# Optimization experiments

Measured on AMD Instinct MI355X. Metric: run time of the kernel, lower is better.

Reference implementation:

```python
import jax, jax.numpy as jnp
import numpy as np

B, W, F, D, H, L = 8, 256, 16, 128, 8, 4
DH = D                      # dim_head = embedding_dims in the original call
INNER = H * DH              # 1024
TIME_EMB = 4
SCALE = DH ** -0.5


def causal_conv(x, w, b, dilation):
    # x: [B, F, W]; w: [F, 1, K] depthwise (groups=F); left-pad (K-1)*dilation -> causal
    k = w.shape[-1]
    pad = (k - 1) * dilation
    y = jax.lax.conv_general_dilated(
        x, w, window_strides=(1,), padding=[(pad, 0)], rhs_dilation=(dilation,),
        dimension_numbers=("NCH", "OIH", "NCH"), feature_group_count=F)
    return y + b[None, :, None]


def sinusoidal_pe(length, d):
    pos = jnp.arange(length, dtype=jnp.float32)[:, None]
    div = jnp.exp(jnp.arange(0, d, 2, dtype=jnp.float32) * (-np.log(10000.0) / d))
    pe = jnp.zeros((length, d), dtype=jnp.float32)
    pe = pe.at[:, 0::2].set(jnp.sin(pos * div)).at[:, 1::2].set(jnp.cos(pos * div))
    return pe  # [W, D]


def layer_norm(x, g, b):
    m = x.mean(-1, keepdims=True)
    v = x.var(-1, keepdims=True)
    return (x - m) * jax.lax.rsqrt(v + 1e-5) * g + b


def vt_attention(x, g, bln, wqkv, wout, bout):
    # x: [B, W, F, D] -> PreNorm then dual-axis (variable + temporal) attention
    h = layer_norm(x, g, bln)
    qkv = h @ wqkv                                   # [B,W,F,3*INNER]
    q, k, v = jnp.split(qkv, 3, axis=-1)
    heads = lambda t: t.reshape(B, W, F, H, DH)
    q, k, v = heads(q) * SCALE, heads(k), heads(v)
    # variable attention: attend across the feature axis (per time step)
    av = jax.nn.softmax(jnp.einsum("bwihe,bwjhe->bwhij", q, k), axis=-1)  # [B,W,H,F,F]
    ov = jnp.einsum("bwhij,bwjhe->bwihe", av, v)
    # temporal attention: attend across the window axis (per variable)
    at = jax.nn.softmax(jnp.einsum("bifhe,bjfhe->bfhij", q, k), axis=-1)  # [B,F,H,W,W]
    ot = jnp.einsum("bfhij,bjfhe->bifhe", at, v)
    o = (ov + ot).reshape(B, W, F, INNER)
    return o @ wout + bout                            # [B,W,F,D]


def setup_inputs() -> dict:
    key = jax.random.key(0)
    ks = jax.random.split(key, 16)
    n = lambda k, shape, sc: jax.random.normal(k, shape, dtype=jnp.float32) * sc
    return {
        "x": jax.random.normal(ks[0], (B, W, F), dtype=jnp.float32),
        "conv_w1": n(ks[1], (F, 1, 4), 0.3), "conv_b1": jnp.zeros((F,), jnp.float32),
        "conv_w2": n(ks[2], (F, 1, 8), 0.2), "conv_b2": jnp.zeros((F,), jnp.float32),
        "conv_w3": n(ks[3], (F, 1, 16), 0.15), "conv_b3": jnp.zeros((F,), jnp.float32),
        "w_val": n(ks[4], (TIME_EMB, D), 0.3), "b_val": jnp.zeros((D,), jnp.float32),
        "ln_g": jnp.ones((L, D), jnp.float32), "ln_b": jnp.zeros((L, D), jnp.float32),
        "w_qkv": n(ks[5], (L, D, 3 * INNER), D ** -0.5),
        "w_out": n(ks[6], (L, INNER, D), INNER ** -0.5),
        "b_out": jnp.zeros((L, D), jnp.float32),
        "w_head": n(ks[7], (F * D, F), (F * D) ** -0.5),
        "b_head": jnp.zeros((F,), jnp.float32),
    }


def reference(x, conv_w1, conv_b1, conv_w2, conv_b2, conv_w3, conv_b3,
              w_val, b_val, ln_g, ln_b, w_qkv, w_out, b_out, w_head, b_head):
    xt = jnp.transpose(x, (0, 2, 1))                  # b w f -> b f w
    c1 = causal_conv(xt, conv_w1, conv_b1, 1)
    c2 = causal_conv(xt, conv_w2, conv_b2, 2)
    c3 = causal_conv(xt, conv_w3, conv_b3, 3)
    s = jnp.stack([xt, c1, c2, c3], axis=-1)          # [B,F,W,4]
    s = jnp.transpose(s, (0, 2, 1, 3))                # [B,W,F,4]
    e = s @ w_val + b_val                             # [B,W,F,D]
    pe = sinusoidal_pe(W, D)                          # [W,D] broadcast over b,f
    h = e + pe[None, :, None, :]
    for l in range(L):
        xo = vt_attention(h, ln_g[l], ln_b[l], w_qkv[l], w_out[l], b_out[l])
        h = xo + h                                    # residual
    out = h.reshape(B, W, F * D) @ w_head + b_head    # [B,W,F]
    return out
```

## Files before the change

kernel.cpp:

```cpp
#include <hip/hip_runtime.h>
#include <hip/hip_bf16.h>
#include <math.h>

#define BB 8
#define WW 256
#define FF 16
#define DD 128
#define HH 8
#define NTOK (BB*WW*FF)
#define SCALE 0.08838834764831845f
#define INV_D (1.0f/128.0f)
#define LN10K_D 0.07195578415606394f

typedef __hip_bfloat16 bf16;
typedef short bf16x8 __attribute__((ext_vector_type(8)));
typedef float f32x4 __attribute__((ext_vector_type(4)));

__device__ __forceinline__ float bf2f(bf16 x){ return __bfloat162float(x); }
__device__ __forceinline__ bf16 f2bf(float x){ return __float2bfloat16(x); }
__device__ __forceinline__ unsigned short bfbits(float x){ bf16 b = f2bf(x); return *(unsigned short*)&b; }
__device__ __forceinline__ float bits2f(unsigned short u){ bf16 b = *(bf16*)&u; return __bfloat162float(b); }

#define MFMA16 __builtin_amdgcn_mfma_f32_16x16x32_bf16


__global__ __launch_bounds__(256) void embed_kernel(
    const float* __restrict__ x,
    const float* __restrict__ w1, const float* __restrict__ b1,
    const float* __restrict__ w2, const float* __restrict__ b2,
    const float* __restrict__ w3, const float* __restrict__ b3,
    const float* __restrict__ wval, const float* __restrict__ bval,
    const float* __restrict__ g, const float* __restrict__ bln,
    float* __restrict__ h, bf16* __restrict__ hn)
{
    int bw = blockIdx.x;
    int b = bw >> 8, w = bw & 255;
    int tid = threadIdx.x;
    __shared__ float s[FF][4];
    __shared__ float hs[16*132];
    if (tid < 64) {
        int f = tid >> 2, t = tid & 3;
        const float* xb = x + (size_t)b*WW*FF + f;
        float v;
        if (t == 0) {
            v = xb[(size_t)w*FF];
        } else if (t == 1) {
            float acc = b1[f];
            #pragma unroll
            for (int kk = 0; kk < 4; kk++) { int t0 = w - (3-kk); if (t0 >= 0) acc += w1[f*4+kk]*xb[(size_t)t0*FF]; }
            v = acc;
        } else if (t == 2) {
            float acc = b2[f];
            #pragma unroll
            for (int kk = 0; kk < 8; kk++) { int t0 = w - (7-kk)*2; if (t0 >= 0) acc += w2[f*8+kk]*xb[(size_t)t0*FF]; }
            v = acc;
        } else {
            float acc = b3[f];
            #pragma unroll
            for (int kk = 0; kk < 16; kk++) { int t0 = w - (15-kk)*3; if (t0 >= 0) acc += w3[f*16+kk]*xb[(size_t)t0*FF]; }
            v = acc;
        }
        s[f][t] = v;
    }
    __syncthreads();
    #pragma unroll
    for (int r = 0; r < 8; r++) {
        int lin = r*256 + tid;
        int f = lin >> 7, d = lin & 127;
        float div = expf(-(float)(d & ~1) * LN10K_D);
        float arg = (float)w * div;
        float pe = (d & 1) ? cosf(arg) : sinf(arg);
        float e = bval[d] + pe;
        #pragma unroll
        for (int t = 0; t < 4; t++) e += s[f][t]*wval[t*128 + d];
        h[((size_t)bw*FF + f)*128 + d] = e;
        hs[f*132 + d] = e;
    }
    __syncthreads();
    int tok = tid >> 4, sub = tid & 15;
    float xv[8];
    #pragma unroll
    for (int e2 = 0; e2 < 8; e2++) xv[e2] = hs[tok*132 + sub*8 + e2];
    float s1 = 0.f, s2 = 0.f;
    #pragma unroll
    for (int e2 = 0; e2 < 8; e2++) { s1 += xv[e2]; s2 += xv[e2]*xv[e2]; }
    #pragma unroll
    for (int m = 1; m < 16; m <<= 1) { s1 += __shfl_xor(s1, m, 64); s2 += __shfl_xor(s2, m, 64); }
    float mean = s1*INV_D;
    float var  = s2*INV_D - mean*mean;
    float rs = rsqrtf(var + 1e-5f);
    union { uint4 u; unsigned short sh[8]; } ou;
    #pragma unroll
    for (int e2 = 0; e2 < 8; e2++) {
        int d = sub*8 + e2;
        ou.sh[e2] = bfbits((xv[e2]-mean)*rs*g[d] + bln[d]);
    }
    *(uint4*)(hn + ((size_t)bw*16 + tok)*128 + sub*8) = ou.u;
}

__global__ __launch_bounds__(256) void transpose_w(
    const float* __restrict__ wqkv, const float* __restrict__ wout,
    const float* __restrict__ wh,
    bf16* __restrict__ wqkvT, bf16* __restrict__ woutT, bf16* __restrict__ whT)
{
    __shared__ float tile[64][65];
    int bx = blockIdx.x, tid = threadIdx.x;
    const float* in; bf16* outp; int r0, c0, sin, sout, nmax;
    if (bx < 384) {
        int l = bx / 96, t = bx % 96;
        r0 = (t / 48)*64; c0 = (t % 48)*64;
        in = wqkv + (size_t)l*128*3072; outp = wqkvT + (size_t)l*3072*128;
        sin = 3072; sout = 128; nmax = 3072;
    } else if (bx < 512) {
        int j = bx - 384, l = j / 32, t = j % 32;
        r0 = (t / 2)*64; c0 = (t % 2)*64;
        in = wout + (size_t)l*1024*128; outp = woutT + (size_t)l*128*1024;
        sin = 128; sout = 1024; nmax = 128;
    } else {
        int t = bx - 512;
        r0 = t*64; c0 = 0;
        in = wh; outp = whT; sin = 16; sout = 2048; nmax = 16;
    }
    int rr = tid >> 2, cg = (tid & 3)*16;
    if (c0 + cg < nmax) {
        const float* src = in + (size_t)(r0 + rr)*sin + c0 + cg;
        #pragma unroll
        for (int i = 0; i < 4; i++)
            *(float4*)&tile[rr][cg + i*4] = *(const float4*)(src + i*4);
    }
    __syncthreads();
    int n = c0 + rr;
    if (n < nmax) {
        union { uint4 u[2]; unsigned short sh[16]; } o;
        #pragma unroll
        for (int e = 0; e < 16; e++) o.sh[e] = bfbits(tile[cg + e][rr]);
        bf16* dst = outp + (size_t)n*sout + r0 + cg;
        *(uint4*)dst = o.u[0];
        *(uint4*)(dst + 8) = o.u[1];
    }
}

__global__ __launch_bounds__(256) void qkv_mfma(
    const bf16* __restrict__ hn, const bf16* __restrict__ wT,
    bf16* __restrict__ q, bf16* __restrict__ k, bf16* __restrict__ v,
    int dummy)
{
    __shared__ __align__(16) unsigned short Cs[4][64][72];
    int tid = threadIdx.x;
    int lane = tid & 63, wave = tid >> 6;
    int quad = lane >> 4, l16 = lane & 15;
    int wm = wave >> 1, wn = wave & 1;
    int m0 = blockIdx.x * 128, n0 = blockIdx.y * 128;

    f32x4 acc[4][4];
    #pragma unroll
    for (int a = 0; a < 4; a++)
        #pragma unroll
        for (int c = 0; c < 4; c++) acc[a][c] = 0.f;

    #pragma unroll
    for (int kt = 0; kt < 4; kt++) {
        int ko = kt*32 + quad*8;
        bf16x8 af[4], bfr[4];
        #pragma unroll
        for (int tm = 0; tm < 4; tm++)
            af[tm] = *(const bf16x8*)(hn + (size_t)(m0 + wm*64 + tm*16 + l16)*128 + ko);
        #pragma unroll
        for (int tn = 0; tn < 4; tn++)
            bfr[tn] = *(const bf16x8*)(wT + (size_t)(n0 + wn*64 + tn*16 + l16)*128 + ko);
        #pragma unroll
        for (int tm = 0; tm < 4; tm++)
            #pragma unroll
            for (int tn = 0; tn < 4; tn++)
                acc[tm][tn] = MFMA16(af[tm], bfr[tn], acc[tm][tn], 0, 0, 0);
    }

    bf16* dst; int nrel; float scl; int isq;
    if (n0 < 1024)      { dst = q; nrel = n0;        scl = SCALE; isq = 1; }
    else if (n0 < 2048) { dst = k; nrel = n0 - 1024; scl = 1.0f;  isq = 0; }
    else                { dst = v; nrel = n0 - 2048; scl = 1.0f;  isq = 0; }

    #pragma unroll
    for (int tm = 0; tm < 4; tm++)
        #pragma unroll
        for (int tn = 0; tn < 4; tn++)
            #pragma unroll
            for (int r = 0; r < 4; r++)
                Cs[wave][tm*16 + quad*4 + r][tn*16 + l16] = bfbits(acc[tm][tn][r]*scl);

    if (isq) {
        #pragma unroll
        for (int p = 0; p < 8; p++) {
            int row = p*8 + (lane >> 3);
            int c8  = (lane & 7)*8;
            uint4 val = *(const uint4*)&Cs[wave][row][c8];
            size_t gaddr = (size_t)(m0 + wm*64 + row)*1024 + nrel + wn*64 + c8;
            *(uint4*)(dst + gaddr) = val;
        }
    } else {
        int hh = nrel >> 7;
        #pragma unroll
        for (int p = 0; p < 8; p++) {
            int row = p*8 + (lane >> 3);
            int c8  = (lane & 7)*8;
            uint4 val = *(const uint4*)&Cs[wave][row][c8];
            int tok = m0 + wm*64 + row;
            int bl = tok >> 12, w = (tok >> 4) & 255, f = tok & 15;
            int d  = wn*64 + c8;
            size_t gaddr = ((size_t)((bl*16 + f)*8 + hh) << 15) + (size_t)w*128 + d;
            *(uint4*)(dst + gaddr) = val;
        }
    }
}

__global__ __launch_bounds__(256) void tattn_mfma(
    const bf16* __restrict__ q, const bf16* __restrict__ k, const bf16* __restrict__ v,
    bf16* __restrict__ o)
{
    __shared__ __align__(16) unsigned short VsT[128*72];
    __shared__ __align__(16) unsigned short Ps[4][16][72];
    unsigned short* Os = VsT;
    unsigned int* VsTdw = (unsigned int*)VsT;

    int bx = blockIdx.x;
    int hh = bx & 7, it2 = (bx>>3) & 1, f = (bx>>4) & 15, bl = bx >> 8;
    int tid = threadIdx.x;
    int lane = tid & 63, wave = tid >> 6;
    int quad = lane >> 4, l16 = lane & 15;

    size_t baseQ = ((size_t)(bl*WW)*FF + f)*1024 + (size_t)hh*128;
    size_t baseK = (size_t)((bl*16 + f)*8 + hh) << 15;

    #pragma unroll 1
    for (int pass = 0; pass < 2; pass++) {
        int i0 = it2*128 + pass*64;

        bf16x8 af[4];
        {
            size_t qa = baseQ + (size_t)(i0 + wave*16 + l16)*16384;
            #pragma unroll
            for (int kt = 0; kt < 4; kt++)
                af[kt] = *(const bf16x8*)(q + qa + kt*32 + quad*8);
        }

        f32x4 oacc[8];
        #pragma unroll
        for (int t = 0; t < 8; t++) oacc[t] = 0.f;
        float m_run[4], l_run[4];
        #pragma unroll
        for (int r = 0; r < 4; r++) { m_run[r] = -1e30f; l_run[r] = 0.f; }

        #pragma unroll 1
        for (int jt = 0; jt < 4; jt++) {
            __syncthreads();
            #pragma unroll
            for (int p = 0; p < 2; p++) {
                int lin = p*256 + tid;
                int j2 = lin & 31;
                int c2 = (lin >> 5)*8;
                union { uint4 u; unsigned short sh[8]; } a, b;
                a.u = *(const uint4*)(v + baseK + (size_t)(jt*64 + 2*j2)*128 + c2);
                b.u = *(const uint4*)(v + baseK + (size_t)(jt*64 + 2*j2 + 1)*128 + c2);
                int col2 = (((2*j2) + (c2 & 56)) & 63) >> 1;
                #pragma unroll
                for (int e = 0; e < 8; e++)
                    VsTdw[(c2+e)*36 + col2] = (unsigned int)a.sh[e] | ((unsigned int)b.sh[e] << 16);
            }
            __syncthreads();

            f32x4 st[4];
            #pragma unroll
            for (int t = 0; t < 4; t++) st[t] = 0.f;
            #pragma unroll
            for (int t = 0; t < 4; t++) {
                size_t ja = baseK + (size_t)(jt*64 + t*16 + l16)*128;
                #pragma unroll
                for (int kt = 0; kt < 4; kt++) {
                    bf16x8 kf = *(const bf16x8*)(k + ja + kt*32 + quad*8);
                    st[t] = MFMA16(af[kt], kf, st[t], 0, 0, 0);
                }
            }

            float tmax[4];
            #pragma unroll
            for (int r = 0; r < 4; r++) tmax[r] = fmaxf(fmaxf(st[0][r], st[1][r]), fmaxf(st[2][r], st[3][r]));
            #pragma unroll
            for (int m = 1; m < 16; m <<= 1)
                #pragma unroll
                for (int r = 0; r < 4; r++) tmax[r] = fmaxf(tmax[r], __shfl_xor(tmax[r], m, 64));
            float alpha[4], rsum[4];
            #pragma unroll
            for (int r = 0; r < 4; r++) {
                float mnew = fmaxf(m_run[r], tmax[r]);
                alpha[r] = __expf(m_run[r] - mnew);
                m_run[r] = mnew;
                rsum[r] = 0.f;
            }
            #pragma unroll
            for (int t = 0; t < 4; t++)
                #pragma unroll
                for (int r = 0; r < 4; r++) {
                    float pp = __expf(st[t][r] - m_run[r]);
                    st[t][r] = pp;
                    rsum[r] += pp;
                }
            #pragma unroll
            for (int m = 1; m < 16; m <<= 1)
                #pragma unroll
                for (int r = 0; r < 4; r++) rsum[r] += __shfl_xor(rsum[r], m, 64);
            #pragma unroll
            for (int r = 0; r < 4; r++) l_run[r] = l_run[r]*alpha[r] + rsum[r];
            #pragma unroll
            for (int t = 0; t < 8; t++)
                #pragma unroll
                for (int r = 0; r < 4; r++) oacc[t][r] *= alpha[r];

            #pragma unroll
            for (int t = 0; t < 4; t++)
                #pragma unroll
                for (int r = 0; r < 4; r++)
                    Ps[wave][quad*4+r][t*16+l16] = bfbits(st[t][r]);

            #pragma unroll
            for (int kt2 = 0; kt2 < 2; kt2++) {
                int kbase = kt2*32 + quad*8;
                bf16x8 pf = *(const bf16x8*)&Ps[wave][l16][kbase];
                #pragma unroll
                for (int t = 0; t < 8; t++) {
                    int d = t*16 + l16;
                    int colstart = (kbase + (((d>>3)&7) << 3)) & 63;
                    bf16x8 vf = *(const bf16x8*)&VsT[d*72 + colstart];
                    oacc[t] = MFMA16(pf, vf, oacc[t], 0, 0, 0);
                }
            }
        }

        __syncthreads();
        float inv[4];
        #pragma unroll
        for (int r = 0; r < 4; r++) inv[r] = 1.f / l_run[r];
        #pragma unroll
        for (int t = 0; t < 8; t++)
            #pragma unroll
            for (int r = 0; r < 4; r++)
                Os[(wave*16 + quad*4 + r)*136 + t*16 + l16] = bfbits(oacc[t][r]*inv[r]);
        __syncthreads();
        #pragma unroll
        for (int r4 = 0; r4 < 4; r4++) {
            int row = r4*4 + quad;
            uint4 val = *(const uint4*)&Os[(wave*16 + row)*136 + l16*8];
            size_t gaddr = baseQ + (size_t)(i0 + wave*16 + row)*16384 + l16*8;
            *(uint4*)(o + gaddr) = val;
        }
    }
}

__global__ __launch_bounds__(256) void vproj_mfma(
    const bf16* __restrict__ q, const bf16* __restrict__ k, const bf16* __restrict__ v,
    const bf16* __restrict__ ot, const bf16* __restrict__ woT,
    const float* __restrict__ bo, float* __restrict__ h,
    bf16* __restrict__ hn, const float* __restrict__ gN, const float* __restrict__ bN,
    int donorm, int tokbase)
{
    __shared__ __align__(16) unsigned short VsT[1024*24];
    __shared__ __align__(16) unsigned short Ps[4][16][24];
    __shared__ float red2[4][16][2];
    unsigned short* Osum = VsT;
    unsigned int* VsTdw = (unsigned int*)VsT;

    int tid = threadIdx.x;
    int lane = tid & 63, wave = tid >> 6, quad = lane >> 4, l16 = lane & 15;
    int bl = blockIdx.x >> 8, w = blockIdx.x & 255;
    size_t base = (size_t)blockIdx.x * 16384;
    size_t woff = (size_t)w * 128;

    uint4 otpre[8];
    #pragma unroll
    for (int u = 0; u < 8; u++) {
        int lin = u*256 + tid;
        int fr = lin >> 7, dc = (lin & 127)*8;
        otpre[u] = *(const uint4*)(ot + base + (size_t)fr*1024 + dc);
    }

    #pragma unroll
    for (int p = 0; p < 4; p++) {
        int lin = p*256 + tid;
        int j2 = lin & 7;
        int d0 = (lin >> 3)*8;
        int hh2 = d0 >> 7, dd = d0 & 127;
        union { uint4 u; unsigned short sh[8]; } a, b;
        a.u = *(const uint4*)(v + (((size_t)((bl*16 + 2*j2  )*8 + hh2)) << 15) + woff + dd);
        b.u = *(const uint4*)(v + (((size_t)((bl*16 + 2*j2+1)*8 + hh2)) << 15) + woff + dd);
        #pragma unroll
        for (int e = 0; e < 8; e++)
            VsTdw[(d0+e)*12 + j2] = (unsigned int)a.sh[e] | ((unsigned int)b.sh[e] << 16);
    }
    __syncthreads();

    bf16x8 zf = {0,0,0,0,0,0,0,0};
    f32x4 oa[2][8];
    #pragma unroll
    for (int hi = 0; hi < 2; hi++) {
        int hh = wave*2 + hi;
        size_t hb = base + hh*128;

        f32x4 s = {0.f,0.f,0.f,0.f};
        size_t ka = (((size_t)((bl*16 + l16)*8 + hh)) << 15) + woff;
        #pragma unroll
        for (int kt = 0; kt < 4; kt++) {
            bf16x8 qf = *(const bf16x8*)(q + hb + (size_t)l16*1024 + kt*32 + quad*8);
            bf16x8 kf = *(const bf16x8*)(k + ka + kt*32 + quad*8);
            s = MFMA16(qf, kf, s, 0, 0, 0);
        }
        float p[4];
        #pragma unroll
        for (int r = 0; r < 4; r++) {
            float mxv = s[r];
            #pragma unroll
            for (int m = 1; m < 16; m <<= 1) mxv = fmaxf(mxv, __shfl_xor(mxv, m, 64));
            float e = __expf(s[r] - mxv);
            float smv = e;
            #pragma unroll
            for (int m = 1; m < 16; m <<= 1) smv += __shfl_xor(smv, m, 64);
            p[r] = e / smv;
        }
        #pragma unroll
        for (int r = 0; r < 4; r++) Ps[wave][quad*4+r][l16] = bfbits(p[r]);

        bf16x8 pf = zf;
        if (quad < 2) pf = *(const bf16x8*)&Ps[wave][l16][quad*8];
        #pragma unroll
        for (int dt = 0; dt < 8; dt++) oa[hi][dt] = 0.f;
        #pragma unroll
        for (int dt = 0; dt < 8; dt++) {
            bf16x8 vf = zf;
            if (quad < 2) vf = *(const bf16x8*)&VsT[(size_t)(hh*128 + dt*16 + l16)*24 + quad*8];
            oa[hi][dt] = MFMA16(pf, vf, oa[hi][dt], 0, 0, 0);
        }
    }

    __syncthreads();
    #pragma unroll
    for (int hi = 0; hi < 2; hi++) {
        int hh = wave*2 + hi;
        #pragma unroll
        for (int dt = 0; dt < 8; dt++)
            #pragma unroll
            for (int r = 0; r < 4; r++)
                Osum[(quad*4 + r)*1048 + hh*128 + dt*16 + l16] = bfbits(oa[hi][dt][r]);
    }
    __syncthreads();

    #pragma unroll
    for (int u = 0; u < 8; u++) {
        int lin = u*256 + tid;
        int fr = lin >> 7, dc = (lin & 127)*8;
        union { uint4 u4; unsigned short sh[8]; } a, bsh, wv;
        a.u4   = otpre[u];
        bsh.u4 = *(const uint4*)&Osum[fr*1048 + dc];
        #pragma unroll
        for (int e = 0; e < 8; e++)
            wv.sh[e] = bfbits(bits2f(a.sh[e]) + bits2f(bsh.sh[e]));
        *(uint4*)&Osum[fr*1048 + dc] = wv.u4;
    }
    __syncthreads();

    f32x4 pacc[2];
    pacc[0] = 0.f; pacc[1] = 0.f;
    #pragma unroll 4
    for (int kt2 = 0; kt2 < 32; kt2++) {
        bf16x8 af2 = *(const bf16x8*)&Osum[l16*1048 + kt2*32 + quad*8];
        #pragma unroll
        for (int nt = 0; nt < 2; nt++) {
            bf16x8 bfr = *(const bf16x8*)(woT + (size_t)(wave*32 + nt*16 + l16)*1024 + kt2*32 + quad*8);
            pacc[nt] = MFMA16(af2, bfr, pacc[nt], 0, 0, 0);
        }
    }

    int htok = tokbase + blockIdx.x*16;
    float hv[2][4];
    #pragma unroll
    for (int nt = 0; nt < 2; nt++) {
        int n = wave*32 + nt*16 + l16;
        float bias = bo[n];
        #pragma unroll
        for (int r = 0; r < 4; r++) {
            size_t idx = (size_t)(htok + quad*4 + r)*128 + n;
            float nv = h[idx] + pacc[nt][r] + bias;
            h[idx] = nv;
            hv[nt][r] = nv;
        }
    }

    if (donorm) {
        float s1[4], s2[4];
        #pragma unroll
        for (int r = 0; r < 4; r++) {
            s1[r] = hv[0][r] + hv[1][r];
            s2[r] = hv[0][r]*hv[0][r] + hv[1][r]*hv[1][r];
        }
        #pragma unroll
        for (int m = 1; m < 16; m <<= 1)
            #pragma unroll
            for (int r = 0; r < 4; r++) {
                s1[r] += __shfl_xor(s1[r], m, 64);
                s2[r] += __shfl_xor(s2[r], m, 64);
            }
        __syncthreads();
        if (l16 == 0) {
            #pragma unroll
            for (int r = 0; r < 4; r++) {
                red2[wave][quad*4+r][0] = s1[r];
                red2[wave][quad*4+r][1] = s2[r];
            }
        }
        __syncthreads();
        #pragma unroll
        for (int nt = 0; nt < 2; nt++) {
            int n = wave*32 + nt*16 + l16;
            float gn = gN[n], bn = bN[n];
            #pragma unroll
            for (int r = 0; r < 4; r++) {
                int t = quad*4 + r;
                float t1 = red2[0][t][0] + red2[1][t][0] + red2[2][t][0] + red2[3][t][0];
                float t2 = red2[0][t][1] + red2[1][t][1] + red2[2][t][1] + red2[3][t][1];
                float mean = t1*INV_D;
                float var  = t2*INV_D - mean*mean;
                float rsv = rsqrtf(var + 1e-5f);
                Osum[t*1048 + n] = bfbits((hv[nt][r]-mean)*rsv*gn + bn);
            }
        }
        __syncthreads();
        int row = tid >> 4, c8 = (tid & 15)*8;
        uint4 val = *(const uint4*)&Osum[row*1048 + c8];
        *(uint4*)(hn + (size_t)(htok + row)*128 + c8) = val;
    }
}

__global__ __launch_bounds__(256) void head_mfma(
    const float* __restrict__ h, const bf16* __restrict__ whT,
    const float* __restrict__ bh, float* __restrict__ out)
{
    __shared__ float sred[4][16][17];
    int tid = threadIdx.x;
    int lane = tid & 63, wave = tid >> 6, quad = lane >> 4, l16 = lane & 15;
    int bw0 = blockIdx.x * 16;
    const float* hrow = h + (size_t)(bw0 + l16)*2048 + wave*512;
    const bf16* wrow  = whT + (size_t)l16*2048 + wave*512;

    f32x4 acc = {0.f,0.f,0.f,0.f};
    #pragma unroll 4
    for (int kc = 0; kc < 16; kc++) {
        int ko = kc*32 + quad*8;
        float4 a0 = *(const float4*)(hrow + ko);
        float4 a1 = *(const float4*)(hrow + ko + 4);
        union { bf16x8 v; unsigned short sh[8]; } ua;
        ua.sh[0]=bfbits(a0.x); ua.sh[1]=bfbits(a0.y); ua.sh[2]=bfbits(a0.z); ua.sh[3]=bfbits(a0.w);
        ua.sh[4]=bfbits(a1.x); ua.sh[5]=bfbits(a1.y); ua.sh[6]=bfbits(a1.z); ua.sh[7]=bfbits(a1.w);
        bf16x8 bv = *(const bf16x8*)(wrow + ko);
        acc = MFMA16(ua.v, bv, acc, 0, 0, 0);
    }
    #pragma unroll
    for (int r = 0; r < 4; r++) sred[wave][quad*4+r][l16] = acc[r];
    __syncthreads();
    int i = tid >> 4, n = tid & 15;
    float s = bh[n] + sred[0][i][n] + sred[1][i][n] + sred[2][i][n] + sred[3][i][n];
    out[(size_t)(bw0 + i)*16 + n] = s;
}

extern "C" void kernel_launch(void* const* d_in, const int* in_sizes, int n_in,
                              void* d_out, int out_size, void* d_ws, size_t ws_size,
                              hipStream_t stream)
{
    const float* x    = (const float*)d_in[0];
    const float* w1   = (const float*)d_in[1];
    const float* b1   = (const float*)d_in[2];
    const float* w2   = (const float*)d_in[3];
    const float* b2   = (const float*)d_in[4];
    const float* w3   = (const float*)d_in[5];
    const float* b3   = (const float*)d_in[6];
    const float* wval = (const float*)d_in[7];
    const float* bval = (const float*)d_in[8];
    const float* lng  = (const float*)d_in[9];
    const float* lnb  = (const float*)d_in[10];
    const float* wqkv = (const float*)d_in[11];
    const float* wout = (const float*)d_in[12];
    const float* bout = (const float*)d_in[13];
    const float* wh   = (const float*)d_in[14];
    const float* bh   = (const float*)d_in[15];
    float* out = (float*)d_out;

    char* ws = (char*)d_ws;
    bf16*  wqkvT = (bf16*)ws;
    bf16*  woutT = (bf16*)(ws + 3145728);
    bf16*  whT   = (bf16*)(ws + 4194304);
    float* h     = (float*)(ws + 4259840);
    bf16*  hn    = (bf16*)(ws + 21037056);
    const size_t qoff = 29425664ull;

    int NBL = 1;
    if      (ws_size >= qoff + 8ull*4ull*8388608ull) NBL = 8;
    else if (ws_size >= qoff + 4ull*4ull*8388608ull) NBL = 4;
    else if (ws_size >= qoff + 2ull*4ull*8388608ull) NBL = 2;
    size_t bsz = (size_t)NBL * 8388608ull;
    bf16* q  = (bf16*)(ws + qoff);
    bf16* kk = (bf16*)(ws + qoff + bsz);
    bf16* vv = (bf16*)(ws + qoff + 2*bsz);
    bf16* oo = (bf16*)(ws + qoff + 3*bsz);

    transpose_w<<<544, 256, 0, stream>>>(wqkv, wout, wh, wqkvT, woutT, whT);
    embed_kernel<<<BB*WW, 256, 0, stream>>>(x, w1,b1, w2,b2, w3,b3, wval, bval,
                                            lng, lnb, h, hn);

    for (int l = 0; l < 4; l++) {
        const bf16* wqT_l = wqkvT + (size_t)l*3072*128;
        const bf16* woT_l = woutT + (size_t)l*128*1024;
        const float* bo_l = bout + l*128;
        int donorm = (l < 3) ? 1 : 0;
        const float* gN = lng + (donorm ? (l+1)*128 : 0);
        const float* bN = lnb + (donorm ? (l+1)*128 : 0);
        for (int bb = 0; bb < BB; bb += NBL) {
            int tokbase = bb*WW*FF;
            qkv_mfma<<<dim3(NBL*32, 24), 256, 0, stream>>>(
                hn + (size_t)tokbase*128, wqT_l, q, kk, vv, 0);
            tattn_mfma<<<NBL*FF*HH*2, 256, 0, stream>>>(q, kk, vv, oo);
            vproj_mfma<<<NBL*WW, 256, 0, stream>>>(q, kk, vv, oo, woT_l,
                                                   bo_l, h, hn, gN, bN,
                                                   donorm, tokbase);
        }
    }

    head_mfma<<<BB*WW/16, 256, 0, stream>>>(h, whT, bh, out);
}
```

Before: 1.729 ms.

## Merge prep kernels, fold log2e into Q scale, tighten LDS and occupancy

Combines the weight-transpose and embedding kernels into one launch, which removes a kernel launch. Q is pre-scaled by SCALE*log2(e) so the softmax can use exp2f in place of __expf. The VsT LDS padding is cut from 24 to 16 elements per row, and a minimum-blocks hint is added to tattn_mfma to raise occupancy. The smaller LDS stride may cause bank conflicts, and the occupancy hint may force register spills.

```diff
diff --git a/kernel.cpp b/kernel.cpp
--- a/kernel.cpp
+++ b/kernel.cpp
@@ -8,7 +8,7 @@
 #define DD 128
 #define HH 8
 #define NTOK (BB*WW*FF)
-#define SCALE 0.08838834764831845f
+#define QSCALE 0.12751745f
 #define INV_D (1.0f/128.0f)
 #define LN10K_D 0.07195578415606394f
 
@@ -24,7 +24,10 @@
 #define MFMA16 __builtin_amdgcn_mfma_f32_16x16x32_bf16
 
 
-__global__ __launch_bounds__(256) void embed_kernel(
+__global__ __launch_bounds__(256) void prep_kernel(
+    const float* __restrict__ wqkv, const float* __restrict__ wout,
+    const float* __restrict__ wh,
+    bf16* __restrict__ wqkvT, bf16* __restrict__ woutT, bf16* __restrict__ whT,
     const float* __restrict__ x,
     const float* __restrict__ w1, const float* __restrict__ b1,
     const float* __restrict__ w2, const float* __restrict__ b2,
@@ -33,11 +36,52 @@
     const float* __restrict__ g, const float* __restrict__ bln,
     float* __restrict__ h, bf16* __restrict__ hn)
 {
-    int bw = blockIdx.x;
+    __shared__ __align__(16) char smem[16640];
+    int tid = threadIdx.x;
+
+    if (blockIdx.x < 544) {
+        float (*tile)[65] = (float(*)[65])smem;
+        int bx = blockIdx.x;
+        const float* in; bf16* outp; int r0, c0, sin, sout, nmax;
+        if (bx < 384) {
+            int l = bx / 96, t = bx % 96;
+            r0 = (t / 48)*64; c0 = (t % 48)*64;
+            in = wqkv + (size_t)l*128*3072; outp = wqkvT + (size_t)l*3072*128;
+            sin = 3072; sout = 128; nmax = 3072;
+        } else if (bx < 512) {
+            int j = bx - 384, l = j / 32, t = j % 32;
+            r0 = (t / 2)*64; c0 = (t % 2)*64;
+            in = wout + (size_t)l*1024*128; outp = woutT + (size_t)l*128*1024;
+            sin = 128; sout = 1024; nmax = 128;
+        } else {
+            int t = bx - 512;
+            r0 = t*64; c0 = 0;
+            in = wh; outp = whT; sin = 16; sout = 2048; nmax = 16;
+        }
+        int rr = tid >> 2, cg = (tid & 3)*16;
+        if (c0 + cg < nmax) {
+            const float* src = in + (size_t)(r0 + rr)*sin + c0 + cg;
+            #pragma unroll
+            for (int i = 0; i < 4; i++)
+                *(float4*)&tile[rr][cg + i*4] = *(const float4*)(src + i*4);
+        }
+        __syncthreads();
+        int n = c0 + rr;
+        if (n < nmax) {
+            union { uint4 u[2]; unsigned short sh[16]; } o;
+            #pragma unroll
+            for (int e = 0; e < 16; e++) o.sh[e] = bfbits(tile[cg + e][rr]);
+            bf16* dst = outp + (size_t)n*sout + r0 + cg;
+            *(uint4*)dst = o.u[0];
+            *(uint4*)(dst + 8) = o.u[1];
+        }
+        return;
+    }
+
+    float (*s)[4] = (float(*)[4])smem;
+    float* hs = (float*)(smem + 256);
+    int bw = blockIdx.x - 544;
     int b = bw >> 8, w = bw & 255;
-    int tid = threadIdx.x;
-    __shared__ float s[FF][4];
-    __shared__ float hs[16*132];
     if (tid < 64) {
         int f = tid >> 2, t = tid & 3;
         const float* xb = x + (size_t)b*WW*FF + f;
@@ -98,52 +142,9 @@
     *(uint4*)(hn + ((size_t)bw*16 + tok)*128 + sub*8) = ou.u;
 }
 
-__global__ __launch_bounds__(256) void transpose_w(
-    const float* __restrict__ wqkv, const float* __restrict__ wout,
-    const float* __restrict__ wh,
-    bf16* __restrict__ wqkvT, bf16* __restrict__ woutT, bf16* __restrict__ whT)
-{
-    __shared__ float tile[64][65];
-    int bx = blockIdx.x, tid = threadIdx.x;
-    const float* in; bf16* outp; int r0, c0, sin, sout, nmax;
-    if (bx < 384) {
-        int l = bx / 96, t = bx % 96;
-        r0 = (t / 48)*64; c0 = (t % 48)*64;
-        in = wqkv + (size_t)l*128*3072; outp = wqkvT + (size_t)l*3072*128;
-        sin = 3072; sout = 128; nmax = 3072;
-    } else if (bx < 512) {
-        int j = bx - 384, l = j / 32, t = j % 32;
-        r0 = (t / 2)*64; c0 = (t % 2)*64;
-        in = wout + (size_t)l*1024*128; outp = woutT + (size_t)l*128*1024;
-        sin = 128; sout = 1024; nmax = 128;
-    } else {
-        int t = bx - 512;
-        r0 = t*64; c0 = 0;
-        in = wh; outp = whT; sin = 16; sout = 2048; nmax = 16;
-    }
-    int rr = tid >> 2, cg = (tid & 3)*16;
-    if (c0 + cg < nmax) {
-        const float* src = in + (size_t)(r0 + rr)*sin + c0 + cg;
-        #pragma unroll
-        for (int i = 0; i < 4; i++)
-            *(float4*)&tile[rr][cg + i*4] = *(const float4*)(src + i*4);
-    }
-    __syncthreads();
-    int n = c0 + rr;
-    if (n < nmax) {
-        union { uint4 u[2]; unsigned short sh[16]; } o;
-        #pragma unroll
-        for (int e = 0; e < 16; e++) o.sh[e] = bfbits(tile[cg + e][rr]);
-        bf16* dst = outp + (size_t)n*sout + r0 + cg;
-        *(uint4*)dst = o.u[0];
-        *(uint4*)(dst + 8) = o.u[1];
-    }
-}
-
 __global__ __launch_bounds__(256) void qkv_mfma(
     const bf16* __restrict__ hn, const bf16* __restrict__ wT,
-    bf16* __restrict__ q, bf16* __restrict__ k, bf16* __restrict__ v,
-    int dummy)
+    bf16* __restrict__ q, bf16* __restrict__ k, bf16* __restrict__ v)
 {
     __shared__ __align__(16) unsigned short Cs[4][64][72];
     int tid = threadIdx.x;
@@ -176,9 +177,9 @@
     }
 
     bf16* dst; int nrel; float scl; int isq;
-    if (n0 < 1024)      { dst = q; nrel = n0;        scl = SCALE; isq = 1; }
-    else if (n0 < 2048) { dst = k; nrel = n0 - 1024; scl = 1.0f;  isq = 0; }
-    else                { dst = v; nrel = n0 - 2048; scl = 1.0f;  isq = 0; }
+    if (n0 < 1024)      { dst = q; nrel = n0;        scl = QSCALE; isq = 1; }
+    else if (n0 < 2048) { dst = k; nrel = n0 - 1024; scl = 1.0f;   isq = 0; }
+    else                { dst = v; nrel = n0 - 2048; scl = 1.0f;   isq = 0; }
 
     #pragma unroll
     for (int tm = 0; tm < 4; tm++)
@@ -213,7 +214,7 @@
     }
 }
 
-__global__ __launch_bounds__(256) void tattn_mfma(
+__global__ __launch_bounds__(256, 5) void tattn_mfma(
     const bf16* __restrict__ q, const bf16* __restrict__ k, const bf16* __restrict__ v,
     bf16* __restrict__ o)
 {
@@ -292,7 +293,7 @@
             #pragma unroll
             for (int r = 0; r < 4; r++) {
                 float mnew = fmaxf(m_run[r], tmax[r]);
-                alpha[r] = __expf(m_run[r] - mnew);
+                alpha[r] = exp2f(m_run[r] - mnew);
                 m_run[r] = mnew;
                 rsum[r] = 0.f;
             }
@@ -300,7 +301,7 @@
             for (int t = 0; t < 4; t++)
                 #pragma unroll
                 for (int r = 0; r < 4; r++) {
-                    float pp = __expf(st[t][r] - m_run[r]);
+                    float pp = exp2f(st[t][r] - m_run[r]);
                     st[t][r] = pp;
                     rsum[r] += pp;
                 }
@@ -362,7 +363,7 @@
     bf16* __restrict__ hn, const float* __restrict__ gN, const float* __restrict__ bN,
     int donorm, int tokbase)
 {
-    __shared__ __align__(16) unsigned short VsT[1024*24];
+    __shared__ __align__(16) unsigned short VsT[16768];
     __shared__ __align__(16) unsigned short Ps[4][16][24];
     __shared__ float red2[4][16][2];
     unsigned short* Osum = VsT;
@@ -393,7 +394,7 @@
         b.u = *(const uint4*)(v + (((size_t)((bl*16 + 2*j2+1)*8 + hh2)) << 15) + woff + dd);
         #pragma unroll
         for (int e = 0; e < 8; e++)
-            VsTdw[(d0+e)*12 + j2] = (unsigned int)a.sh[e] | ((unsigned int)b.sh[e] << 16);
+            VsTdw[(d0+e)*8 + j2] = (unsigned int)a.sh[e] | ((unsigned int)b.sh[e] << 16);
     }
     __syncthreads();
 
@@ -418,7 +419,7 @@
             float mxv = s[r];
             #pragma unroll
             for (int m = 1; m < 16; m <<= 1) mxv = fmaxf(mxv, __shfl_xor(mxv, m, 64));
-            float e = __expf(s[r] - mxv);
+            float e = exp2f(s[r] - mxv);
             float smv = e;
             #pragma unroll
             for (int m = 1; m < 16; m <<= 1) smv += __shfl_xor(smv, m, 64);
@@ -434,7 +435,7 @@
         #pragma unroll
         for (int dt = 0; dt < 8; dt++) {
             bf16x8 vf = zf;
-            if (quad < 2) vf = *(const bf16x8*)&VsT[(size_t)(hh*128 + dt*16 + l16)*24 + quad*8];
+            if (quad < 2) vf = *(const bf16x8*)&VsT[(size_t)(hh*128 + dt*16 + l16)*16 + quad*8];
             oa[hi][dt] = MFMA16(pf, vf, oa[hi][dt], 0, 0, 0);
         }
     }
@@ -608,9 +609,9 @@
     bf16* vv = (bf16*)(ws + qoff + 2*bsz);
     bf16* oo = (bf16*)(ws + qoff + 3*bsz);
 
-    transpose_w<<<544, 256, 0, stream>>>(wqkv, wout, wh, wqkvT, woutT, whT);
-    embed_kernel<<<BB*WW, 256, 0, stream>>>(x, w1,b1, w2,b2, w3,b3, wval, bval,
-                                            lng, lnb, h, hn);
+    prep_kernel<<<544 + BB*WW, 256, 0, stream>>>(
+        wqkv, wout, wh, wqkvT, woutT, whT,
+        x, w1,b1, w2,b2, w3,b3, wval, bval, lng, lnb, h, hn);
 
     for (int l = 0; l < 4; l++) {
         const bf16* wqT_l = wqkvT + (size_t)l*3072*128;
@@ -622,7 +623,7 @@
         for (int bb = 0; bb < BB; bb += NBL) {
             int tokbase = bb*WW*FF;
             qkv_mfma<<<dim3(NBL*32, 24), 256, 0, stream>>>(
-                hn + (size_t)tokbase*128, wqT_l, q, kk, vv, 0);
+                hn + (size_t)tokbase*128, wqT_l, q, kk, vv);
             tattn_mfma<<<NBL*FF*HH*2, 256, 0, stream>>>(q, kk, vv, oo);
             vproj_mfma<<<NBL*WW, 256, 0, stream>>>(q, kk, vv, oo, woT_l,
                                                    bo_l, h, hn, gN, bN,
```

Measured after the change: 1.823 ms. +5.5%, slower.
